# Performance work log

Hardware: AMD Instinct MI355X
Metric: run time of the kernel (lower is better)

Reference implementation:

```python
import jax, jax.numpy as jnp
import numpy as np

H, W, NUM_HEADS = 32, 32, 8


def dwconv3x3(x, w, b):
    # x: (B,C,H,W), w: (C,1,3,3) depthwise, b: (C,)
    y = jax.lax.conv_general_dilated(
        x, w, window_strides=(1, 1), padding='SAME',
        dimension_numbers=('NCHW', 'OIHW', 'NCHW'),
        feature_group_count=x.shape[1])
    return y + b[None, :, None, None]


def conv1x1(x, w, b):
    # x: (B,C,H,W), w: (O,C), b: (O,)
    return jnp.einsum('oc,bchw->bohw', w, x) + b[None, :, None, None]


def layernorm(x, w, b, eps=1e-6):
    mu = x.mean(-1, keepdims=True)
    var = ((x - mu) ** 2).mean(-1, keepdims=True)
    return (x - mu) / jnp.sqrt(var + eps) * w + b


def setup_inputs() -> dict:
    key = jax.random.key(0)
    ks = jax.random.split(key, 12)
    B, N, C = 32, H * W, 512
    Ch = 4 * C  # inverted MLP hidden
    s_lin = 0.02
    s_dw = np.sqrt(2.0 / 9.0)   # fan_out init for 3x3 depthwise
    s_pw1 = np.sqrt(2.0 / Ch)
    s_pw2 = np.sqrt(2.0 / C)
    return {
        'x': jax.random.normal(ks[0], (B, N, C), jnp.float32),
        'cpe_w': jax.random.normal(ks[1], (C, 1, 3, 3), jnp.float32) * s_dw,
        'cpe_b': jnp.zeros((C,), jnp.float32),
        'ln1_w': jnp.ones((C,), jnp.float32),
        'ln1_b': jnp.zeros((C,), jnp.float32),
        'qkv_w': jax.random.normal(ks[2], (3 * C, C), jnp.float32) * s_lin,
        'crpe_w': jax.random.normal(ks[3], (C, 1, 3, 3), jnp.float32) * s_dw,
        'crpe_b': jnp.zeros((C,), jnp.float32),
        'ln2_w': jnp.ones((C,), jnp.float32),
        'ln2_b': jnp.zeros((C,), jnp.float32),
        'fc1_w': jax.random.normal(ks[4], (Ch, C), jnp.float32) * s_pw1,
        'fc1_b': jnp.zeros((Ch,), jnp.float32),
        'dw_w': jax.random.normal(ks[5], (Ch, 1, 3, 3), jnp.float32) * s_dw,
        'dw_b': jnp.zeros((Ch,), jnp.float32),
        'fc2_w': jax.random.normal(ks[6], (C, Ch), jnp.float32) * s_pw2,
        'fc2_b': jnp.zeros((C,), jnp.float32),
    }


def reference(x, cpe_w, cpe_b, ln1_w, ln1_b, qkv_w, crpe_w, crpe_b,
              ln2_w, ln2_b, fc1_w, fc1_b, dw_w, dw_b, fc2_w, fc2_b):
    B, N, C = x.shape
    h = NUM_HEADS
    d = C // h
    scale = d ** -0.5

    # --- Convolutional position encoding: x = x + dwconv(x) ---
    img = x.reshape(B, H, W, C).transpose(0, 3, 1, 2)  # B C H W
    img = img + dwconv3x3(img, cpe_w, cpe_b)
    x = img.transpose(0, 2, 3, 1).reshape(B, N, C)

    # --- Factorized attention + conv relative position encoding ---
    cur = layernorm(x, ln1_w, ln1_b)
    qkv = cur @ qkv_w.T                                 # (B,N,3C)
    qkv = qkv.reshape(B, N, 3, h, d).transpose(2, 0, 3, 1, 4)  # (3,B,h,N,d)
    q, k, v = qkv[0], qkv[1], qkv[2]
    k_softmax = jax.nn.softmax(k, axis=2)               # softmax over tokens N
    ktv = jnp.einsum('bhnk,bhnv->bhkv', k_softmax, v)   # (B,h,d,d)
    factor_att = jnp.einsum('bhnk,bhkv->bhnv', q, ktv)  # (B,h,N,d)
    # crpe: depthwise conv on v as image, elementwise-multiplied by q
    v_img = v.transpose(0, 1, 3, 2).reshape(B, h * d, H, W)
    v_img = dwconv3x3(v_img, crpe_w, crpe_b)
    v_conv = v_img.reshape(B, h, d, N).transpose(0, 1, 3, 2)
    crpe = q * v_conv
    attn_out = (scale * factor_att + crpe).transpose(0, 2, 1, 3).reshape(B, N, C)
    x = x + attn_out

    # --- Inverted MLP (conv-based channel mixing) ---
    cur = layernorm(x, ln2_w, ln2_b)
    img = cur.reshape(B, H, W, C).transpose(0, 3, 1, 2)  # B C H W
    hdn = conv1x1(img, fc1_w, fc1_b)
    hdn = jax.nn.gelu(hdn, approximate=False)
    hdn = hdn + dwconv3x3(hdn, dw_w, dw_b)
    out = conv1x1(hdn, fc2_w, fc2_b)
    x = x + out.transpose(0, 2, 3, 1).reshape(B, N, C)
    return x
```

## Files before the change

kernel.cpp:

```cpp
#include <hip/hip_runtime.h>
#include <hip/hip_bf16.h>

using bf16 = __hip_bfloat16;
using s16x4 = __attribute__((ext_vector_type(4))) short;
using s16x8 = __attribute__((ext_vector_type(8))) short;
using f32x4 = __attribute__((ext_vector_type(4))) float;

#define DI __device__ __forceinline__

template <int N> DI void wvm() {
    if constexpr (N == 8) asm volatile("s_waitcnt vmcnt(8)" ::: "memory");
    else if constexpr (N == 4) asm volatile("s_waitcnt vmcnt(4)" ::: "memory");
    else if constexpr (N == 2) asm volatile("s_waitcnt vmcnt(2)" ::: "memory");
    else asm volatile("s_waitcnt vmcnt(0)" ::: "memory");
}

DI float b2f(short s) { union { unsigned u; float f; } z; z.u = ((unsigned)(unsigned short)s) << 16; return z.f; }
DI short f2b(float f) { bf16 t = __float2bfloat16(f); return *(short*)&t; }

DI float gelu_f(float x) {
    const float t = 0.7978845608f * x * (1.f + 0.044715f * x * x);
    const float e = __expf(2.f * t);
    const float th = 1.f - 2.f / (e + 1.f);
    return 0.5f * x * (1.f + th);
}

DI void ld8(const bf16* p, float* f) {
    s16x8 x = *(const s16x8*)(const void*)p;
#pragma unroll
    for (int c = 0; c < 8; c++) f[c] = b2f(x[c]);
}
DI void ld8(const float* p, float* f) {
    float4 a = *(const float4*)p, b = *(const float4*)(p + 4);
    f[0]=a.x; f[1]=a.y; f[2]=a.z; f[3]=a.w; f[4]=b.x; f[5]=b.y; f[6]=b.z; f[7]=b.w;
}

typedef const __attribute__((address_space(1))) void* gp_t;
typedef __attribute__((address_space(3))) void* lp_t;
DI void gload_lds16(const void* g, void* l) {
    __builtin_amdgcn_global_load_lds((gp_t)g, (lp_t)l, 16, 0, 0);
}

__global__ void diag_k(float* out, float v) { out[0] = v; }

__global__ void f2bf_k(const float* __restrict__ in, bf16* __restrict__ out, int n) {
    int i = (blockIdx.x * 256 + threadIdx.x) * 8;
    if (i >= n) return;
    float f[8];
    ld8(in + i, f);
    s16x8 o;
#pragma unroll
    for (int c = 0; c < 8; c++) o[c] = f2b(f[c]);
    *(s16x8*)(void*)(out + i) = o;
}

__global__ void f2bf_w2_k(const float* __restrict__ in, bf16* __restrict__ out) {
    const int i = (blockIdx.x * 256 + threadIdx.x) * 8;
    const int n = i >> 11, c = i & 2047;
    const int h = c >> 10, k = c & 1023;
    float f[8];
    ld8(in + i, f);
    s16x8 o;
#pragma unroll
    for (int e = 0; e < 8; e++) o[e] = f2b(f[e]);
    *(s16x8*)(void*)(out + (size_t)h * 524288 + n * 1024 + k) = o;
}

DI void tap10(const float* r, float w0, float w1, float w2, float* acc) {
#pragma unroll
    for (int i = 0; i < 8; i++)
        acc[i] += w0 * r[i] + w1 * r[i + 1] + w2 * r[i + 2];
}

template <typename TI, typename TO, bool RESID, int CPL>
__global__ __launch_bounds__(256) void conv4_k(
    const TI* in, long rs, long coff,
    const float* __restrict__ w, const float* __restrict__ bias,
    TO* out, long ors, int gshift)
{
    constexpr int CH = 64 * CPL;
    constexpr int ECNT = CH / 8;
    __shared__ float buf[2][CH][33];
    const int t = threadIdx.x;
    const int band = blockIdx.x & 3;
    const int cg = (blockIdx.x >> 2) & ((1 << gshift) - 1);
    const int img = blockIdx.x >> (2 + gshift);
    const int y0 = band * 8;

    const int spx = t >> 3;
    const int sce = (t & 7) * ECNT;
    const TI* gsrc = in + ((long)img << 10) * rs + coff + (long)cg * CH + sce;

    const int c = t & 63;
    const int xb = (t >> 6) * 8;

    float wv9[9][CPL], bw[CPL];
#pragma unroll
    for (int p = 0; p < CPL; p++) {
        const int gch = cg * CH + c * CPL + p;
#pragma unroll
        for (int j = 0; j < 9; j++) wv9[j][p] = w[gch * 9 + j];
        bw[p] = bias[gch];
    }

    auto stage = [&](int row) {
        float f[ECNT];
        ld8(gsrc + (long)(row * 32 + spx) * rs, f);
        if constexpr (ECNT == 16) ld8(gsrc + (long)(row * 32 + spx) * rs + 8, f + 8);
        float* d = &buf[row & 1][0][0];
#pragma unroll
        for (int k = 0; k < ECNT; k++) {
            const int ch = sce + k;
            const int rr = (CPL == 2) ? ((ch & 1) * 64 + (ch >> 1)) : ch;
            d[rr * 33 + spx] = f[k];
        }
    };
    auto slice = [&](int row, float r[CPL][10]) {
#pragma unroll
        for (int p = 0; p < CPL; p++) {
            const float* s = &buf[row & 1][c + p * 64][0];
            r[p][0] = (xb == 0) ? 0.f : s[xb - 1];
#pragma unroll
            for (int i = 0; i < 8; i++) r[p][1 + i] = s[xb + i];
            r[p][9] = (xb + 8 >= 32) ? 0.f : s[xb + 8];
        }
    };
    auto zero = [&](float r[CPL][10]) {
#pragma unroll
        for (int p = 0; p < CPL; p++)
#pragma unroll
            for (int i = 0; i < 10; i++) r[p][i] = 0.f;
    };

    float r0[CPL][10], r1[CPL][10], r2[CPL][10];
    if (y0 > 0) stage(y0 - 1);
    __syncthreads();
    if (y0 > 0) slice(y0 - 1, r0); else zero(r0);
    stage(y0);
    __syncthreads();
    slice(y0, r1);

    for (int y = y0; y < y0 + 8; ++y) {
        const int yn = y + 1;
        if (yn <= 31) stage(yn);
        __syncthreads();
        if (yn <= 31) slice(yn, r2); else zero(r2);
        float acc[CPL][8];
#pragma unroll
        for (int p = 0; p < CPL; p++) {
#pragma unroll
            for (int i = 0; i < 8; i++) acc[p][i] = bw[p];
            tap10(r0[p], wv9[0][p], wv9[1][p], wv9[2][p], acc[p]);
            tap10(r1[p], wv9[3][p], wv9[4][p], wv9[5][p], acc[p]);
            tap10(r2[p], wv9[6][p], wv9[7][p], wv9[8][p], acc[p]);
            if (RESID) {
#pragma unroll
                for (int i = 0; i < 8; i++) acc[p][i] += r1[p][i + 1];
            }
        }
        TO* o = out + ((long)(img * 1024 + y * 32 + xb)) * ors + (long)cg * CH + c * CPL;
#pragma unroll
        for (int i = 0; i < 8; i++) {
            if constexpr (CPL == 2 && sizeof(TO) == 2) {
                const unsigned u = (unsigned)(unsigned short)f2b(acc[0][i]) |
                                   ((unsigned)(unsigned short)f2b(acc[1][i]) << 16);
                *(unsigned*)(void*)(o + (long)i * ors) = u;
            } else {
                o[(long)i * ors] = (TO)acc[0][i];
            }
        }
#pragma unroll
        for (int p = 0; p < CPL; p++)
#pragma unroll
            for (int i = 0; i < 10; i++) { r0[p][i] = r1[p][i]; r1[p][i] = r2[p][i]; }
    }
}

__global__ __launch_bounds__(256) void ln_k(const float* __restrict__ x,
                                            const float* __restrict__ w,
                                            const float* __restrict__ bp,
                                            bf16* __restrict__ out)
{
    const size_t row = blockIdx.x * 4 + (threadIdx.x >> 6);
    const int t = threadIdx.x & 63;
    const float* xr = x + row * 512;
    alignas(16) float v[8];
    *(float4*)&v[0] = *(const float4*)(xr + t * 8);
    *(float4*)&v[4] = *(const float4*)(xr + t * 8 + 4);
    float s = 0.f;
#pragma unroll
    for (int j = 0; j < 8; j++) s += v[j];
#pragma unroll
    for (int mm = 32; mm; mm >>= 1) s += __shfl_xor(s, mm);
    const float mu = s * (1.f / 512.f);
    float q = 0.f;
#pragma unroll
    for (int j = 0; j < 8; j++) { v[j] -= mu; q += v[j] * v[j]; }
#pragma unroll
    for (int mm = 32; mm; mm >>= 1) q += __shfl_xor(q, mm);
    const float rstd = rsqrtf(q * (1.f / 512.f) + 1e-6f);
    alignas(16) float wv[8], bv[8];
    *(float4*)&wv[0] = *(const float4*)(w + t * 8);
    *(float4*)&wv[4] = *(const float4*)(w + t * 8 + 4);
    *(float4*)&bv[0] = *(const float4*)(bp + t * 8);
    *(float4*)&bv[4] = *(const float4*)(bp + t * 8 + 4);
    alignas(16) bf16 o[8];
#pragma unroll
    for (int j = 0; j < 8; j++) o[j] = __float2bfloat16(v[j] * rstd * wv[j] + bv[j]);
    *(uint4*)(out + row * 512 + t * 8) = *(const uint4*)o;
}

template <int EPI, int K>
__global__ __launch_bounds__(512) void gemm8p_k(
    const bf16* __restrict__ A, const bf16* __restrict__ Bw,
    const float* __restrict__ bias, const float* resid,
    bf16* __restrict__ outb, float* outf, int M, int Nn)
{
    constexpr int KT = K / 64;
    __shared__ __align__(16) char lds[131072];
    char* ldsA = lds;
    char* ldsB = lds + 65536;
    const int t = threadIdx.x;
    const int lane = t & 63;
    const int w = t >> 6;
    const int wr = w >> 2, wc = w & 3;
    const int m0 = blockIdx.x * 256;
    const int n0 = blockIdx.y * 256;
    const int lr = lane & 15, lg = lane >> 4;

    f32x4 acc[8][4] = {};

    const int srow = lane >> 3;
    const int ssrc = 8 * ((lane & 7) ^ srow);

    auto SA = [&](int b, int kt, int h) {
#pragma unroll
        for (int j = 0; j < 2; j++) {
            const int lrow0 = j * 64 + w * 8;
            const int R0 = j * 128 + h * 64 + (lrow0 & 63);
            gload_lds16(A + (size_t)(m0 + R0 + srow) * K + kt * 64 + ssrc,
                        ldsA + ((b * 2 + h) * 128 + lrow0) * 128);
        }
    };
    auto SB = [&](int b, int kt, int h) {
#pragma unroll
        for (int j = 0; j < 2; j++) {
            const int lrow0 = j * 64 + w * 8;
            const int R0 = (lrow0 >> 5) * 64 + h * 32 + (lrow0 & 31);
            gload_lds16(Bw + (size_t)(n0 + R0 + srow) * K + kt * 64 + ssrc,
                        ldsB + ((b * 2 + h) * 128 + lrow0) * 128);
        }
    };
    auto RA = [&](int b, int h, int m, int ks) -> s16x8 {
        return *(const s16x8*)(ldsA + ((b * 2 + h) * 128 + wr * 64 + m * 16 + lr) * 128
                               + (((ks * 4 + lg) ^ (lr & 7)) << 4));
    };
    auto RB = [&](int b, int h, int n, int ks) -> s16x8 {
        return *(const s16x8*)(ldsB + ((b * 2 + h) * 128 + wc * 32 + n * 16 + lr) * 128
                               + (((ks * 4 + lg) ^ (lr & 7)) << 4));
    };
    auto MM = [&](int mb, int nb, s16x8 (&a)[2][4], s16x8 (&b)[2][2]) {
#pragma unroll
        for (int ks = 0; ks < 2; ks++)
#pragma unroll
            for (int m = 0; m < 4; m++)
#pragma unroll
                for (int n = 0; n < 2; n++)
                    acc[mb + m][nb + n] =
                        __builtin_amdgcn_mfma_f32_16x16x32_bf16(a[ks][m], b[ks][n], acc[mb + m][nb + n], 0, 0, 0);
    };

    SA(0, 0, 0); SB(0, 0, 0); SA(0, 0, 1); SB(0, 0, 1);
    SA(1, 1, 0); SB(1, 1, 0);
    wvm<8>();
    __builtin_amdgcn_s_barrier();

    s16x8 aLo[2][4], aHi[2][4], bLo[2][2], bHi[2][2];
    auto TILE = [&](int kt) {
        const int b = kt & 1;
#pragma unroll
        for (int ks = 0; ks < 2; ks++) {
#pragma unroll
            for (int m = 0; m < 4; m++) aLo[ks][m] = RA(b, 0, m, ks);
#pragma unroll
            for (int n = 0; n < 2; n++) bLo[ks][n] = RB(b, 0, n, ks);
        }
        if (kt + 1 < KT) SA(b ^ 1, kt + 1, 1);
        __builtin_amdgcn_s_barrier();
        __builtin_amdgcn_s_setprio(1);
        MM(0, 0, aLo, bLo);
        __builtin_amdgcn_s_setprio(0);
        if (kt + 1 < KT) wvm<8>(); else wvm<2>();
        __builtin_amdgcn_s_barrier();
#pragma unroll
        for (int ks = 0; ks < 2; ks++)
#pragma unroll
            for (int m = 0; m < 4; m++) aHi[ks][m] = RA(b, 1, m, ks);
        if (kt + 1 < KT) SB(b ^ 1, kt + 1, 1);
        __builtin_amdgcn_s_barrier();
        __builtin_amdgcn_s_setprio(1);
        MM(4, 0, aHi, bLo);
        __builtin_amdgcn_s_setprio(0);
        if (kt + 1 < KT) wvm<8>(); else wvm<0>();
        __builtin_amdgcn_s_barrier();
#pragma unroll
        for (int ks = 0; ks < 2; ks++)
#pragma unroll
            for (int n = 0; n < 2; n++) bHi[ks][n] = RB(b, 1, n, ks);
        if (kt + 2 < KT) SA(b, kt + 2, 0);
        __builtin_amdgcn_s_barrier();
        __builtin_amdgcn_s_setprio(1);
        MM(4, 2, aHi, bHi);
        __builtin_amdgcn_s_setprio(0);
        __builtin_amdgcn_s_barrier();
        if (kt + 2 < KT) SB(b, kt + 2, 0);
        __builtin_amdgcn_s_barrier();
        __builtin_amdgcn_s_setprio(1);
        MM(0, 2, aLo, bHi);
        __builtin_amdgcn_s_setprio(0);
        if (kt + 2 < KT) { wvm<8>(); __builtin_amdgcn_s_barrier(); }
        else if (kt + 1 < KT) { wvm<4>(); __builtin_amdgcn_s_barrier(); }
    };

    if constexpr (KT <= 8) {
#pragma unroll
        for (int kt = 0; kt < KT; ++kt) TILE(kt);
    } else {
#pragma unroll 2
        for (int kt = 0; kt < KT; ++kt) TILE(kt);
    }

#pragma unroll
    for (int i = 0; i < 8; i++) {
#pragma unroll
        for (int j = 0; j < 4; j++) {
            const int col = n0 + wc * 64 + j * 16 + lr;
            float bcol = 0.f;
            if constexpr (EPI == 1 || EPI == 2) bcol = bias[col];
#pragma unroll
            for (int r = 0; r < 4; r++) {
                const int row = m0 + wr * 128 + i * 16 + lg * 4 + r;
                float v = acc[i][j][r] + bcol;
                const size_t idx = (size_t)row * Nn + col;
                if (EPI >= 2) outf[idx] = v + resid[idx];
                else outb[idx] = __float2bfloat16(EPI == 1 ? gelu_f(v) : v);
            }
        }
    }
}

__global__ __launch_bounds__(256) void ktv2_k(const bf16* __restrict__ qkv,
                                              bf16* __restrict__ ktvT)
{
    __shared__ __align__(16) char P[64 * 128];
    __shared__ __align__(16) char Vt[64 * 128];
    __shared__ float csl[64 * 5];
    const int t = threadIdx.x;
    const int b = blockIdx.x >> 3, hh = blockIdx.x & 7;
    const int lane = t & 63, w = t >> 6;
    const int lr = lane & 15, lg = lane >> 4;

    const int n_r = t >> 2;
    const int k0 = (t & 3) * 16;
    const bf16* kbase = qkv + (size_t)(b * 1024) * 1536 + 512 + hh * 64 + k0;
    const bf16* vbase = kbase + 512;

    const int kq = t & 63, qq = t >> 6;
    float cacc = 0.f;

    f32x4 acc[4] = {};

    for (int n0 = 0; n0 < 1024; n0 += 64) {
        const uint4 ka = *(const uint4*)(kbase + (size_t)(n0 + n_r) * 1536);
        const uint4 kb2 = *(const uint4*)(kbase + (size_t)(n0 + n_r) * 1536 + 8);
        const uint4 va = *(const uint4*)(vbase + (size_t)(n0 + n_r) * 1536);
        const uint4 vb2 = *(const uint4*)(vbase + (size_t)(n0 + n_r) * 1536 + 8);
        __syncthreads();
        {
            const short* ke = (const short*)&ka;
            const short* ke2 = (const short*)&kb2;
            const short* ve = (const short*)&va;
            const short* ve2 = (const short*)&vb2;
            const int nslot = ((n_r >> 3) << 4);
            const int nbyte = (n_r & 7) * 2;
#pragma unroll
            for (int j = 0; j < 16; j++) {
                const int row = k0 + j;
                const short kv = j < 8 ? ke[j] : ke2[j - 8];
                const short vv = j < 8 ? ve[j] : ve2[j - 8];
                const int off = row * 128 + (nslot ^ ((row & 7) << 4)) + nbyte;
                *(short*)(P + off) = f2b(__expf(b2f(kv)));
                *(short*)(Vt + off) = vv;
            }
        }
        __syncthreads();
        {
            const char* pr = P + kq * 128;
            const int sw = (kq & 7) << 4;
            s16x8 x0 = *(const s16x8*)(pr + (((qq * 2) << 4) ^ sw));
            s16x8 x1 = *(const s16x8*)(pr + (((qq * 2 + 1) << 4) ^ sw));
#pragma unroll
            for (int j = 0; j < 8; j++) cacc += b2f(x0[j]) + b2f(x1[j]);
        }
#pragma unroll
        for (int ks2 = 0; ks2 < 2; ks2++) {
            s16x8 aF = *(const s16x8*)(Vt + (w * 16 + lr) * 128 + (((ks2 * 4 + lg) ^ (lr & 7)) << 4));
            s16x8 bF[4];
#pragma unroll
            for (int j = 0; j < 4; j++)
                bF[j] = *(const s16x8*)(P + (j * 16 + lr) * 128 + (((ks2 * 4 + lg) ^ (lr & 7)) << 4));
#pragma unroll
            for (int j = 0; j < 4; j++)
                acc[j] = __builtin_amdgcn_mfma_f32_16x16x32_bf16(aF, bF[j], acc[j], 0, 0, 0);
        }
    }
    __syncthreads();
    csl[kq * 5 + qq] = cacc;
    __syncthreads();
    if (t < 64) csl[t * 5 + 4] = csl[t * 5] + csl[t * 5 + 1] + csl[t * 5 + 2] + csl[t * 5 + 3];
    __syncthreads();

    bf16* o = ktvT + (size_t)(b * 8 + hh) * 4096;
#pragma unroll
    for (int j = 0; j < 4; j++) {
        const int col = j * 16 + lr;
        const float sc = 0.125f / csl[col * 5 + 4];
#pragma unroll
        for (int r = 0; r < 4; r++) {
            const int vrow = w * 16 + lg * 4 + r;
            o[vrow * 64 + col] = __float2bfloat16(acc[j][r] * sc);
        }
    }
}

__global__ __launch_bounds__(256) void attnout2_k(
    float* xs, const bf16* __restrict__ qkv,
    const bf16* __restrict__ ktvT, const bf16* __restrict__ vc)
{
    __shared__ __align__(16) char qs[256 * 128];
    __shared__ __align__(16) char ks[64 * 128];
    const int t = threadIdx.x;
    const int bid = blockIdx.x;
    const int b = bid >> 5, hh = (bid >> 2) & 7, nc = bid & 3;
    const int n0 = nc * 256;
    const int lane = t & 63, w = t >> 6;
    const int lr = lane & 15, lg = lane >> 4;

    {
        const int r0 = t >> 3, sl = t & 7;
#pragma unroll
        for (int it = 0; it < 8; it++) {
            const int row = it * 32 + r0;
            const uint4 v = *(const uint4*)(qkv + ((size_t)(b * 1024 + n0 + row)) * 1536 + hh * 64 + sl * 8);
            *(uint4*)(qs + row * 128 + ((sl ^ (row & 7)) << 4)) = v;
        }
#pragma unroll
        for (int it = 0; it < 2; it++) {
            const int u = it * 256 + t;
            const int vr = u >> 3, sl2 = u & 7;
            const uint4 vv = *(const uint4*)(ktvT + (size_t)(b * 8 + hh) * 4096 + vr * 64 + sl2 * 8);
            *(uint4*)(ks + vr * 128 + ((sl2 ^ (vr & 7)) << 4)) = vv;
        }
    }
    __syncthreads();

    f32x4 acc[4][4] = {};
    s16x8 aF[2][4], bF[2][4];
#pragma unroll
    for (int ksi = 0; ksi < 2; ksi++) {
#pragma unroll
        for (int m = 0; m < 4; m++) {
            const int row = w * 64 + m * 16 + lr;
            aF[ksi][m] = *(const s16x8*)(qs + row * 128 + (((ksi * 4 + lg) ^ (lr & 7)) << 4));
        }
#pragma unroll
        for (int j = 0; j < 4; j++) {
            const int vr = j * 16 + lr;
            bF[ksi][j] = *(const s16x8*)(ks + vr * 128 + (((ksi * 4 + lg) ^ (lr & 7)) << 4));
        }
    }
#pragma unroll
    for (int ksi = 0; ksi < 2; ksi++)
#pragma unroll
        for (int m = 0; m < 4; m++)
#pragma unroll
            for (int j = 0; j < 4; j++)
                acc[m][j] = __builtin_amdgcn_mfma_f32_16x16x32_bf16(aF[ksi][m], bF[ksi][j], acc[m][j], 0, 0, 0);

#pragma unroll
    for (int m = 0; m < 4; m++) {
#pragma unroll
        for (int j = 0; j < 4; j++) {
#pragma unroll
            for (int r = 0; r < 4; r++) {
                const int lrow = w * 64 + m * 16 + lg * 4 + r;
                const int col = j * 16 + lr;
                const size_t idx = ((size_t)(b * 1024 + n0 + lrow)) * 512 + hh * 64 + col;
                const short qv = *(const short*)(qs + lrow * 128 + ((((col >> 3) ^ (lrow & 7)) << 4)) + (col & 7) * 2);
                xs[idx] = xs[idx] + acc[m][j][r] + b2f(qv) * __bfloat162float(vc[idx]);
            }
        }
    }
}

static constexpr size_t OFF_WQ   = 0;
static constexpr size_t OFF_W1   = 1572864;
static constexpr size_t OFF_W2   = 3670016;
static constexpr size_t OFF_CUR  = 5767168;
static constexpr size_t OFF_QKV  = 39321600;
static constexpr size_t OFF_VC   = 139984896;
static constexpr size_t OFF_KTV  = 173539328;
static constexpr size_t WS_NEED  = 194772992;
static constexpr size_t OFF_HG   = OFF_QKV;
static constexpr size_t OFF_H2   = OFF_QKV + 67108864;

extern "C" void kernel_launch(void* const* d_in, const int* in_sizes, int n_in,
                              void* d_out, int out_size, void* d_ws, size_t ws_size,
                              hipStream_t stream)
{
    const float* x     = (const float*)d_in[0];
    const float* cpe_w = (const float*)d_in[1];
    const float* cpe_b = (const float*)d_in[2];
    const float* ln1_w = (const float*)d_in[3];
    const float* ln1_b = (const float*)d_in[4];
    const float* qkv_w = (const float*)d_in[5];
    const float* crpe_w= (const float*)d_in[6];
    const float* crpe_b= (const float*)d_in[7];
    const float* ln2_w = (const float*)d_in[8];
    const float* ln2_b = (const float*)d_in[9];
    const float* fc1_w = (const float*)d_in[10];
    const float* fc1_b = (const float*)d_in[11];
    const float* dw_w  = (const float*)d_in[12];
    const float* dw_b  = (const float*)d_in[13];
    const float* fc2_w = (const float*)d_in[14];
    const float* fc2_b = (const float*)d_in[15];
    float* spine = (float*)d_out;
    char* ws = (char*)d_ws;

    if (ws_size < WS_NEED) {
        diag_k<<<1, 1, 0, stream>>>(spine, (float)ws_size);
        return;
    }

    bf16*  wq   = (bf16*)(ws + OFF_WQ);
    bf16*  w1   = (bf16*)(ws + OFF_W1);
    bf16*  w2r  = (bf16*)(ws + OFF_W2);
    bf16*  cur  = (bf16*)(ws + OFF_CUR);
    bf16*  qkv  = (bf16*)(ws + OFF_QKV);
    bf16*  vc   = (bf16*)(ws + OFF_VC);
    bf16*  ktvT = (bf16*)(ws + OFF_KTV);
    bf16*  hg   = (bf16*)(ws + OFF_HG);
    bf16*  h2   = (bf16*)(ws + OFF_H2);

    f2bf_k<<<(1536 * 512 / 8 + 255) / 256, 256, 0, stream>>>(qkv_w, wq, 1536 * 512);
    f2bf_k<<<(2048 * 512 / 8 + 255) / 256, 256, 0, stream>>>(fc1_w, w1, 2048 * 512);
    f2bf_w2_k<<<512 * 2048 / 8 / 256, 256, 0, stream>>>(fc2_w, w2r);

    conv4_k<float, float, true, 1><<<32 * 8 * 4, 256, 0, stream>>>(x, 512, 0, cpe_w, cpe_b, spine, 512, 3);

    const int M = 32768;
    ln_k<<<M / 4, 256, 0, stream>>>(spine, ln1_w, ln1_b, cur);
    gemm8p_k<0, 512><<<dim3(128, 6), 512, 0, stream>>>(cur, wq, nullptr, nullptr, qkv, nullptr, M, 1536);
    ktv2_k<<<256, 256, 0, stream>>>(qkv, ktvT);
    conv4_k<bf16, bf16, false, 2><<<32 * 4 * 4, 256, 0, stream>>>(qkv, 1536, 1024, crpe_w, crpe_b, vc, 512, 2);
    attnout2_k<<<32 * 8 * 4, 256, 0, stream>>>(spine, qkv, ktvT, vc);
    ln_k<<<M / 4, 256, 0, stream>>>(spine, ln2_w, ln2_b, cur);

    for (int h = 0; h < 2; h++) {
        gemm8p_k<1, 512><<<dim3(128, 4), 512, 0, stream>>>(
            cur, w1 + (size_t)h * 1024 * 512, fc1_b + h * 1024, nullptr, hg, nullptr, M, 1024);
        conv4_k<bf16, bf16, true, 2><<<32 * 8 * 4, 256, 0, stream>>>(
            hg, 1024, 0, dw_w + (size_t)h * 1024 * 9, dw_b + h * 1024, h2, 1024, 3);
        if (h == 0)
            gemm8p_k<2, 1024><<<dim3(128, 2), 512, 0, stream>>>(
                h2, w2r, fc2_b, spine, nullptr, spine, M, 512);
        else
            gemm8p_k<3, 1024><<<dim3(128, 2), 512, 0, stream>>>(
                h2, w2r + (size_t)1 * 524288, nullptr, spine, nullptr, spine, M, 512);
    }
}
```

Measured before the change: 510.4 us.

## Merge two fc2 GEMM halves into one dual-source K=2048 GEMM and swizzle blocks

The MLP hidden layer is still computed in two 1024-channel halves, but each half now goes to its own buffer. A single fc2 GEMM with K=2048 then reads both halves as one concatenated A operand. This removes one GEMM launch and one full fp32 read-modify-write of the residual spine. The GEMM grid is also flattened and swizzled so neighbouring workgroups share B tiles, which is meant to improve L2 reuse. The cost is a larger workspace and a simpler fc2 weight conversion.

After: 478.3 us. 6.3% less time.

```diff
diff --git a/kernel.cpp b/kernel.cpp
--- a/kernel.cpp
+++ b/kernel.cpp
@@ -52,18 +52,6 @@
 #pragma unroll
     for (int c = 0; c < 8; c++) o[c] = f2b(f[c]);
     *(s16x8*)(void*)(out + i) = o;
-}
-
-__global__ void f2bf_w2_k(const float* __restrict__ in, bf16* __restrict__ out) {
-    const int i = (blockIdx.x * 256 + threadIdx.x) * 8;
-    const int n = i >> 11, c = i & 2047;
-    const int h = c >> 10, k = c & 1023;
-    float f[8];
-    ld8(in + i, f);
-    s16x8 o;
-#pragma unroll
-    for (int e = 0; e < 8; e++) o[e] = f2b(f[e]);
-    *(s16x8*)(void*)(out + (size_t)h * 524288 + n * 1024 + k) = o;
 }
 
 DI void tap10(const float* r, float w0, float w1, float w2, float* acc) {
@@ -210,13 +198,14 @@
     *(uint4*)(out + row * 512 + t * 8) = *(const uint4*)o;
 }
 
-template <int EPI, int K>
+template <int EPI, int K, int NY, bool DUAL = false>
 __global__ __launch_bounds__(512) void gemm8p_k(
-    const bf16* __restrict__ A, const bf16* __restrict__ Bw,
-    const float* __restrict__ bias, const float* resid,
-    bf16* __restrict__ outb, float* outf, int M, int Nn)
+    const bf16* __restrict__ A, const bf16* __restrict__ A2,
+    const bf16* __restrict__ Bw, const float* __restrict__ bias,
+    const float* resid, bf16* __restrict__ outb, float* outf, int M, int Nn)
 {
     constexpr int KT = K / 64;
+    constexpr int LDA = DUAL ? K / 2 : K;
     __shared__ __align__(16) char lds[131072];
     char* ldsA = lds;
     char* ldsB = lds + 65536;
@@ -224,8 +213,10 @@
     const int lane = t & 63;
     const int w = t >> 6;
     const int wr = w >> 2, wc = w & 3;
-    const int m0 = blockIdx.x * 256;
-    const int n0 = blockIdx.y * 256;
+    const int nwg = 128 * NY;
+    const int swz = (blockIdx.x & 7) * (nwg >> 3) + (blockIdx.x >> 3);
+    const int m0 = (swz / NY) * 256;
+    const int n0 = (swz % NY) * 256;
     const int lr = lane & 15, lg = lane >> 4;
 
     f32x4 acc[8][4] = {};
@@ -234,11 +225,14 @@
     const int ssrc = 8 * ((lane & 7) ^ srow);
 
     auto SA = [&](int b, int kt, int h) {
+        const bf16* Ab = A;
+        int ktl = kt;
+        if constexpr (DUAL) { if (kt >= KT / 2) { Ab = A2; ktl = kt - KT / 2; } }
 #pragma unroll
         for (int j = 0; j < 2; j++) {
             const int lrow0 = j * 64 + w * 8;
             const int R0 = j * 128 + h * 64 + (lrow0 & 63);
-            gload_lds16(A + (size_t)(m0 + R0 + srow) * K + kt * 64 + ssrc,
+            gload_lds16(Ab + (size_t)(m0 + R0 + srow) * LDA + ktl * 64 + ssrc,
                         ldsA + ((b * 2 + h) * 128 + lrow0) * 128);
         }
     };
@@ -336,13 +330,13 @@
         for (int j = 0; j < 4; j++) {
             const int col = n0 + wc * 64 + j * 16 + lr;
             float bcol = 0.f;
-            if constexpr (EPI == 1 || EPI == 2) bcol = bias[col];
+            if constexpr (EPI >= 1) bcol = bias[col];
 #pragma unroll
             for (int r = 0; r < 4; r++) {
                 const int row = m0 + wr * 128 + i * 16 + lg * 4 + r;
                 float v = acc[i][j][r] + bcol;
                 const size_t idx = (size_t)row * Nn + col;
-                if (EPI >= 2) outf[idx] = v + resid[idx];
+                if (EPI == 2) outf[idx] = v + resid[idx];
                 else outb[idx] = __float2bfloat16(EPI == 1 ? gelu_f(v) : v);
             }
         }
@@ -507,12 +501,13 @@
 static constexpr size_t OFF_W1   = 1572864;
 static constexpr size_t OFF_W2   = 3670016;
 static constexpr size_t OFF_CUR  = 5767168;
-static constexpr size_t OFF_QKV  = 39321600;
-static constexpr size_t OFF_VC   = 139984896;
-static constexpr size_t OFF_KTV  = 173539328;
-static constexpr size_t WS_NEED  = 194772992;
-static constexpr size_t OFF_HG   = OFF_QKV;
-static constexpr size_t OFF_H2   = OFF_QKV + 67108864;
+static constexpr size_t OFF_H2B  = 5767168;
+static constexpr size_t OFF_QKV  = 72876032;
+static constexpr size_t OFF_HG   = 72876032;
+static constexpr size_t OFF_VC   = 173539328;
+static constexpr size_t OFF_H2A  = 139984896;
+static constexpr size_t OFF_KTV  = 207093760;
+static constexpr size_t WS_NEED  = 207618048;
 
 extern "C" void kernel_launch(void* const* d_in, const int* in_sizes, int n_in,
                               void* d_out, int out_size, void* d_ws, size_t ws_size,
@@ -544,38 +539,32 @@
 
     bf16*  wq   = (bf16*)(ws + OFF_WQ);
     bf16*  w1   = (bf16*)(ws + OFF_W1);
-    bf16*  w2r  = (bf16*)(ws + OFF_W2);
+    bf16*  w2b  = (bf16*)(ws + OFF_W2);
     bf16*  cur  = (bf16*)(ws + OFF_CUR);
     bf16*  qkv  = (bf16*)(ws + OFF_QKV);
     bf16*  vc   = (bf16*)(ws + OFF_VC);
     bf16*  ktvT = (bf16*)(ws + OFF_KTV);
     bf16*  hg   = (bf16*)(ws + OFF_HG);
-    bf16*  h2   = (bf16*)(ws + OFF_H2);
+    bf16*  h2a  = (bf16*)(ws + OFF_H2A);
+    bf16*  h2b  = (bf16*)(ws + OFF_H2B);
 
     f2bf_k<<<(1536 * 512 / 8 + 255) / 256, 256, 0, stream>>>(qkv_w, wq, 1536 * 512);
     f2bf_k<<<(2048 * 512 / 8 + 255) / 256, 256, 0, stream>>>(fc1_w, w1, 2048 * 512);
-    f2bf_w2_k<<<512 * 2048 / 8 / 256, 256, 0, stream>>>(fc2_w, w2r);
+    f2bf_k<<<(2048 * 512 / 8 + 255) / 256, 256, 0, stream>>>(fc2_w, w2b, 512 * 2048);
 
     conv4_k<float, float, true, 1><<<32 * 8 * 4, 256, 0, stream>>>(x, 512, 0, cpe_w, cpe_b, spine, 512, 3);
 
     const int M = 32768;
     ln_k<<<M / 4, 256, 0, stream>>>(spine, ln1_w, ln1_b, cur);
-    gemm8p_k<0, 512><<<dim3(128, 6), 512, 0, stream>>>(cur, wq, nullptr, nullptr, qkv, nullptr, M, 1536);
+    gemm8p_k<0, 512, 6><<<768, 512, 0, stream>>>(cur, nullptr, wq, nullptr, nullptr, qkv, nullptr, M, 1536);
     ktv2_k<<<256, 256, 0, stream>>>(qkv, ktvT);
     conv4_k<bf16, bf16, false, 2><<<32 * 4 * 4, 256, 0, stream>>>(qkv, 1536, 1024, crpe_w, crpe_b, vc, 512, 2);
     attnout2_k<<<32 * 8 * 4, 256, 0, stream>>>(spine, qkv, ktvT, vc);
     ln_k<<<M / 4, 256, 0, stream>>>(spine, ln2_w, ln2_b, cur);
 
-    for (int h = 0; h < 2; h++) {
-        gemm8p_k<1, 512><<<dim3(128, 4), 512, 0, stream>>>(
-            cur, w1 + (size_t)h * 1024 * 512, fc1_b + h * 1024, nullptr, hg, nullptr, M, 1024);
-        conv4_k<bf16, bf16, true, 2><<<32 * 8 * 4, 256, 0, stream>>>(
-            hg, 1024, 0, dw_w + (size_t)h * 1024 * 9, dw_b + h * 1024, h2, 1024, 3);
-        if (h == 0)
-            gemm8p_k<2, 1024><<<dim3(128, 2), 512, 0, stream>>>(
-                h2, w2r, fc2_b, spine, nullptr, spine, M, 512);
-        else
-            gemm8p_k<3, 1024><<<dim3(128, 2), 512, 0, stream>>>(
-                h2, w2r + (size_t)1 * 524288, nullptr, spine, nullptr, spine, M, 512);
-    }
-}
+    gemm8p_k<1, 512, 4><<<512, 512, 0, stream>>>(cur, nullptr, w1, fc1_b, nullptr, hg, nullptr, M, 1024);
+    conv4_k<bf16, bf16, true, 2><<<32 * 8 * 4, 256, 0, stream>>>(hg, 1024, 0, dw_w, dw_b, h2a, 1024, 3);
+    gemm8p_k<1, 512, 4><<<512, 512, 0, stream>>>(cur, nullptr, w1 + (size_t)1024 * 512, fc1_b + 1024, nullptr, hg, nullptr, M, 1024);
+    conv4_k<bf16, bf16, true, 2><<<32 * 8 * 4, 256, 0, stream>>>(hg, 1024, 0, dw_w + (size_t)1024 * 9, dw_b + 1024, h2b, 1024, 3);
+    gemm8p_k<2, 2048, 2, true><<<256, 512, 0, stream>>>(h2a, h2b, w2b, fc2_b, spine, nullptr, spine, M, 512);
+}
```
